# Kernel tuning notes

Hardware: AMD Instinct MI355X
Metric: run time of the kernel (lower is better)

The kernel has to match this reference:

```python
import jax, jax.numpy as jnp
import numpy as np

NUM_ROUTES, NUM_TIME, DIM, K, C = 100000, 2016, 256, 100, 5
BATCH = 262144


def _xavier(key, shape):
    fan_in, fan_out = shape[0], shape[1]
    lim = np.sqrt(6.0 / (fan_in + fan_out))
    return jax.random.uniform(key, shape, jnp.float32, -lim, lim)


def setup_inputs() -> dict:
    key = jax.random.key(0)
    ks = jax.random.split(key, 9)
    route_idx = jax.random.randint(ks[0], (BATCH,), 0, NUM_ROUTES)
    time_idx = jax.random.randint(ks[1], (BATCH,), 0, NUM_TIME)
    route_table = _xavier(ks[2], (NUM_ROUTES, DIM))
    time_table = _xavier(ks[3], (NUM_TIME, DIM))
    w = _xavier(ks[4], (DIM, K))
    mode_a = _xavier(ks[5], (DIM, C))
    mode_b = _xavier(ks[6], (DIM, C))
    mode_bias = jnp.zeros((C, C), jnp.float32)
    fc_lim = 1.0 / np.sqrt(C * C + K)
    fc_w = jax.random.uniform(ks[7], (C * C + K, 1), jnp.float32, -fc_lim, fc_lim)
    fc_b = jax.random.uniform(ks[8], (1,), jnp.float32, -fc_lim, fc_lim)
    return {
        "route_idx": route_idx, "time_idx": time_idx,
        "route_table": route_table, "time_table": time_table,
        "w": w, "mode_a": mode_a, "mode_b": mode_b,
        "mode_bias": mode_bias, "fc_w": fc_w, "fc_b": fc_b,
    }


def reference(route_idx, time_idx, route_table, time_table, w, mode_a, mode_b, mode_bias, fc_w, fc_b):
    r = route_table[route_idx]            # [B, D]
    t = time_table[time_idx]              # [B, D]
    gcp = jax.nn.relu((r * t) @ w)        # [B, K]
    # einsum('ni,nj->nij') then contracting i with mode_a and j with mode_b
    # equals outer product of the two small projections (exact same math):
    ra = r @ mode_a                       # [B, C]
    tb = t @ mode_b                       # [B, C]
    inter = jax.nn.sigmoid(ra[:, :, None] * tb[:, None, :] + mode_bias)  # [B, C, C]
    feats = jnp.concatenate([gcp, inter.reshape(inter.shape[0], -1)], axis=1)  # [B, K + C*C]
    out = feats @ fc_w + fc_b             # [B, 1]
    return jnp.squeeze(out, axis=-1)      # [B]
```

## Files before the change

### kernel.cpp

```cpp
#include <hip/hip_runtime.h>
#include <stdint.h>

#define BATCH   262144
#define NROUTES 100000
#define NTIME   2016
#define DIM     256
#define KOUT    100
#define NTILES  7

typedef __attribute__((ext_vector_type(8))) short bf16x8;
typedef __attribute__((ext_vector_type(4))) float f32x4;

#define WS_W_BYTES  (NTILES * 8 * 64 * 16)
#define WS_RA_OFF   ((size_t)WS_W_BYTES)
#define WS_TB_OFF   (WS_RA_OFF + (size_t)NROUTES * 32)
#define WS_RT16_OFF (WS_TB_OFF + (size_t)NTIME * 32)
#define WS_TT16_OFF (WS_RT16_OFF + (size_t)NROUTES * 512)
#define WS_NEED     (WS_TT16_OFF + (size_t)NTIME * 512)

static __device__ __forceinline__ uint32_t rne_bf16(float f) {
  uint32_t u = __builtin_bit_cast(uint32_t, f);
  u += 0x7FFFu + ((u >> 16) & 1u);
  return u >> 16;
}
static __device__ __forceinline__ uint32_t pk_rne(float a, float b) {
  return rne_bf16(a) | (rne_bf16(b) << 16);
}
static __device__ __forceinline__ uint32_t pk_trunc(float a, float b) {
  return __builtin_amdgcn_perm(__builtin_bit_cast(uint32_t, b),
                               __builtin_bit_cast(uint32_t, a), 0x07060302u);
}
static __device__ __forceinline__ uint32_t mulpk(uint32_t a, uint32_t b) {
  float alo = __builtin_bit_cast(float, a << 16);
  float blo = __builtin_bit_cast(float, b << 16);
  float ahi = __builtin_bit_cast(float, a & 0xFFFF0000u);
  float bhi = __builtin_bit_cast(float, b & 0xFFFF0000u);
  return __builtin_amdgcn_perm(__builtin_bit_cast(uint32_t, ahi * bhi),
                               __builtin_bit_cast(uint32_t, alo * blo), 0x07060302u);
}

__global__ __launch_bounds__(256) void prep_kernel(
    const float* __restrict__ route_table,
    const float* __restrict__ time_table,
    const float* __restrict__ w,
    const float* __restrict__ mode_a,
    const float* __restrict__ mode_b,
    uint8_t* __restrict__ ws, int do16)
{
  const int b   = blockIdx.x;
  const int tid = threadIdx.x;

  if (b < 14) {
    const int u = b * 256 + tid;
    const int lane = u & 63;
    const int frag = u >> 6;
    const int ks = frag / NTILES;
    const int nt = frag % NTILES;
    const int n  = nt * 16 + (lane & 15);
    const int k0 = ks * 32 + (lane >> 4) * 8;
    uint32_t pk[4];
    #pragma unroll
    for (int p = 0; p < 4; ++p) {
      float v0 = (n < KOUT) ? w[(size_t)(k0 + 2 * p) * KOUT + n] : 0.0f;
      float v1 = (n < KOUT) ? w[(size_t)(k0 + 2 * p + 1) * KOUT + n] : 0.0f;
      pk[p] = pk_rne(v0, v1);
    }
    ((uint4*)ws)[u] = make_uint4(pk[0], pk[1], pk[2], pk[3]);
    return;
  }

  const float* tab; const float* proj; float* outp; uint8_t* out16; int base;
  if (b < 14 + 126) {
    tab = time_table;  proj = mode_b; outp = (float*)(ws + WS_TB_OFF);
    out16 = ws + WS_TT16_OFF; base = (b - 14) * 16;
  } else {
    tab = route_table; proj = mode_a; outp = (float*)(ws + WS_RA_OFF);
    out16 = ws + WS_RT16_OFF; base = (b - 140) * 16;
  }

  const int wave = tid >> 6, lane = tid & 63;
  float A[4][5];
  #pragma unroll
  for (int j = 0; j < 4; ++j)
    #pragma unroll
    for (int i = 0; i < 5; ++i)
      A[j][i] = proj[(4 * lane + j) * 5 + i];

  const int row0 = base + wave * 4;
  float4 v[4];
  #pragma unroll
  for (int rr = 0; rr < 4; ++rr)
    v[rr] = *(const float4*)(tab + (size_t)(row0 + rr) * DIM + 4 * lane);

  #pragma unroll
  for (int rr = 0; rr < 4; ++rr) {
    const int row = row0 + rr;
    if (do16) {
      uint2 o;
      o.x = pk_rne(v[rr].x, v[rr].y);
      o.y = pk_rne(v[rr].z, v[rr].w);
      *(uint2*)(out16 + (size_t)row * 512 + lane * 8) = o;
    }
    float p[5];
    #pragma unroll
    for (int i = 0; i < 5; ++i)
      p[i] = v[rr].x * A[0][i] + v[rr].y * A[1][i] + v[rr].z * A[2][i] + v[rr].w * A[3][i];
    #pragma unroll
    for (int off = 32; off >= 1; off >>= 1)
      #pragma unroll
      for (int i = 0; i < 5; ++i)
        p[i] += __shfl_xor(p[i], off, 64);
    if (lane == 0) {
      float* o = outp + (size_t)row * 8;
      o[0] = p[0]; o[1] = p[1]; o[2] = p[2]; o[3] = p[3]; o[4] = p[4];
    }
  }
}

template<int TAB16>
__global__ __launch_bounds__(256, 3) void main_kernel(
    const int*   __restrict__ route_idx,
    const int*   __restrict__ time_idx,
    const float* __restrict__ route_table,
    const float* __restrict__ time_table,
    const float* __restrict__ mode_bias,
    const float* __restrict__ fc_w,
    const float* __restrict__ fc_b,
    const uint8_t* __restrict__ ws,
    float* __restrict__ out)
{
  __shared__ float yg[64];
  const int tid  = threadIdx.x;
  const int wave = tid >> 6, lane = tid & 63;
  const int col  = lane & 15, quad = lane >> 4;
  const int m0   = blockIdx.x * 64 + wave * 16;
  const size_t ri = (size_t)route_idx[m0 + col];
  const size_t ti = (size_t)time_idx[m0 + col];

  uint4 rw[8], tw[8];
  if (TAB16) {
    const uint8_t* rb = ws + WS_RT16_OFF + ri * 512 + quad * 16;
    const uint8_t* tb = ws + WS_TT16_OFF + ti * 512 + quad * 16;
    #pragma unroll
    for (int ks = 0; ks < 8; ++ks) {
      rw[ks] = *(const uint4*)(rb + ks * 64);
      tw[ks] = *(const uint4*)(tb + ks * 64);
    }
  }

  f32x4 acc[NTILES];
  #pragma unroll
  for (int nt = 0; nt < NTILES; ++nt) acc[nt] = (f32x4){0.f, 0.f, 0.f, 0.f};
  const bf16x8* wfr = (const bf16x8*)ws;

  #pragma unroll
  for (int ks = 0; ks < 8; ++ks) {
    uint4 p;
    if (TAB16) {
      p.x = mulpk(rw[ks].x, tw[ks].x);
      p.y = mulpk(rw[ks].y, tw[ks].y);
      p.z = mulpk(rw[ks].z, tw[ks].z);
      p.w = mulpk(rw[ks].w, tw[ks].w);
    } else {
      const float4* rp = (const float4*)(route_table + ri * DIM + ks * 32 + quad * 8);
      const float4* tp = (const float4*)(time_table  + ti * DIM + ks * 32 + quad * 8);
      float4 r0 = rp[0], r1 = rp[1], t0 = tp[0], t1 = tp[1];
      p.x = pk_trunc(r0.x * t0.x, r0.y * t0.y);
      p.y = pk_trunc(r0.z * t0.z, r0.w * t0.w);
      p.z = pk_trunc(r1.x * t1.x, r1.y * t1.y);
      p.w = pk_trunc(r1.z * t1.z, r1.w * t1.w);
    }
    const bf16x8 a = __builtin_bit_cast(bf16x8, p);
    #pragma unroll
    for (int nt = 0; nt < NTILES; ++nt)
      acc[nt] = __builtin_amdgcn_mfma_f32_16x16x32_bf16(a, wfr[(ks * NTILES + nt) * 64 + lane],
                                                        acc[nt], 0, 0, 0);
  }

  float fcw_l[NTILES];
  #pragma unroll
  for (int nt = 0; nt < NTILES; ++nt) {
    const int n = nt * 16 + col;
    fcw_l[nt] = (n < KOUT) ? fc_w[n] : 0.0f;
  }
  #pragma unroll
  for (int reg = 0; reg < 4; ++reg) {
    float s = 0.f;
    #pragma unroll
    for (int nt = 0; nt < NTILES; ++nt)
      s += fmaxf(acc[nt][reg], 0.f) * fcw_l[nt];
    #pragma unroll
    for (int off = 1; off < 16; off <<= 1)
      s += __shfl_xor(s, off, 64);
    if (col == 0) yg[wave * 16 + quad * 4 + reg] = s;
  }
  __syncthreads();

  if (tid < 64) {
    const int n = blockIdx.x * 64 + tid;
    const size_t ri2 = (size_t)route_idx[n];
    const size_t ti2 = (size_t)time_idx[n];
    const float* ra = (const float*)(ws + WS_RA_OFF) + ri2 * 8;
    const float* tb = (const float*)(ws + WS_TB_OFF) + ti2 * 8;
    float rav[5], tbv[5];
    #pragma unroll
    for (int i = 0; i < 5; ++i) { rav[i] = ra[i]; tbv[i] = tb[i]; }
    float o = fc_b[0] + yg[tid];
    #pragma unroll
    for (int i = 0; i < 5; ++i)
      #pragma unroll
      for (int j = 0; j < 5; ++j) {
        const float z  = rav[i] * tbv[j] + mode_bias[i * 5 + j];
        const float sg = 1.0f / (1.0f + __expf(-z));
        o += sg * fc_w[KOUT + i * 5 + j];
      }
    out[n] = o;
  }
}

extern "C" void kernel_launch(void* const* d_in, const int* in_sizes, int n_in,
                              void* d_out, int out_size, void* d_ws, size_t ws_size,
                              hipStream_t stream)
{
  const int*   route_idx   = (const int*)d_in[0];
  const int*   time_idx    = (const int*)d_in[1];
  const float* route_table = (const float*)d_in[2];
  const float* time_table  = (const float*)d_in[3];
  const float* w           = (const float*)d_in[4];
  const float* mode_a      = (const float*)d_in[5];
  const float* mode_b      = (const float*)d_in[6];
  const float* mode_bias   = (const float*)d_in[7];
  const float* fc_w        = (const float*)d_in[8];
  const float* fc_b        = (const float*)d_in[9];
  uint8_t* ws  = (uint8_t*)d_ws;
  float*   out = (float*)d_out;

  const int big = (ws_size >= WS_NEED) ? 1 : 0;

  prep_kernel<<<6390, 256, 0, stream>>>(route_table, time_table, w,
                                        mode_a, mode_b, ws, big);
  if (big)
    main_kernel<1><<<BATCH / 64, 256, 0, stream>>>(route_idx, time_idx,
                                                   route_table, time_table,
                                                   mode_bias, fc_w, fc_b, ws, out);
  else
    main_kernel<0><<<BATCH / 64, 256, 0, stream>>>(route_idx, time_idx,
                                                   route_table, time_table,
                                                   mode_bias, fc_w, fc_b, ws, out);
}
```

Measured before the change: 245.4 us.

## Switch embedding tables and GEMM to FP8 MFMA, drop LDS epilogue

Prep now converts the weight fragments and both embedding tables to scaled FP8 instead of bf16, halving the gathered bytes per row. The main kernel multiplies the FP8 route and time values in f32, requantizes the product to FP8 and uses the fp8 MFMA; fc_w is prescaled to undo the scale factor. The per-row sigmoid interaction epilogue is moved into designated lanes of each wave with DPP reductions, removing shared memory and the block barrier, and occupancy is raised to 4 blocks. Reductions in prep also use DPP. The main risks are FP8 accuracy loss against the tolerance and extra conversion ALU work.

Measured after the change: 225.5 us. 1.09x faster.

```diff
diff --git a/kernel.cpp b/kernel.cpp
--- a/kernel.cpp
+++ b/kernel.cpp
@@ -8,35 +8,36 @@
 #define KOUT    100
 #define NTILES  7
 
-typedef __attribute__((ext_vector_type(8))) short bf16x8;
+typedef __attribute__((ext_vector_type(2))) float f32x2;
 typedef __attribute__((ext_vector_type(4))) float f32x4;
 
-#define WS_W_BYTES  (NTILES * 8 * 64 * 16)
-#define WS_RA_OFF   ((size_t)WS_W_BYTES)
+#define WS_WFRAG_BYTES ((size_t)(NTILES * 8 * 64 * 8))
+#define WS_RA_OFF   (WS_WFRAG_BYTES)
 #define WS_TB_OFF   (WS_RA_OFF + (size_t)NROUTES * 32)
-#define WS_RT16_OFF (WS_TB_OFF + (size_t)NTIME * 32)
-#define WS_TT16_OFF (WS_RT16_OFF + (size_t)NROUTES * 512)
-#define WS_NEED     (WS_TT16_OFF + (size_t)NTIME * 512)
-
-static __device__ __forceinline__ uint32_t rne_bf16(float f) {
-  uint32_t u = __builtin_bit_cast(uint32_t, f);
-  u += 0x7FFFu + ((u >> 16) & 1u);
-  return u >> 16;
-}
-static __device__ __forceinline__ uint32_t pk_rne(float a, float b) {
-  return rne_bf16(a) | (rne_bf16(b) << 16);
-}
-static __device__ __forceinline__ uint32_t pk_trunc(float a, float b) {
-  return __builtin_amdgcn_perm(__builtin_bit_cast(uint32_t, b),
-                               __builtin_bit_cast(uint32_t, a), 0x07060302u);
-}
-static __device__ __forceinline__ uint32_t mulpk(uint32_t a, uint32_t b) {
-  float alo = __builtin_bit_cast(float, a << 16);
-  float blo = __builtin_bit_cast(float, b << 16);
-  float ahi = __builtin_bit_cast(float, a & 0xFFFF0000u);
-  float bhi = __builtin_bit_cast(float, b & 0xFFFF0000u);
-  return __builtin_amdgcn_perm(__builtin_bit_cast(uint32_t, ahi * bhi),
-                               __builtin_bit_cast(uint32_t, alo * blo), 0x07060302u);
+#define WS_RT8_OFF  (WS_TB_OFF + (size_t)NTIME * 32)
+#define WS_TT8_OFF  (WS_RT8_OFF + (size_t)NROUTES * 256)
+#define WS_NEED     (WS_TT8_OFF + (size_t)NTIME * 256)
+
+template<int CTRL>
+static __device__ __forceinline__ float dpp_add(float x) {
+  int s = __builtin_amdgcn_update_dpp(0, __builtin_bit_cast(int, x), CTRL, 0xF, 0xF, true);
+  return x + __builtin_bit_cast(float, s);
+}
+static __device__ __forceinline__ float wave_sum63(float x) {
+  x = dpp_add<0x111>(x);
+  x = dpp_add<0x112>(x);
+  x = dpp_add<0x114>(x);
+  x = dpp_add<0x118>(x);
+  x = dpp_add<0x142>(x);
+  x = dpp_add<0x143>(x);
+  return x;
+}
+static __device__ __forceinline__ float sum16_all(float x) {
+  x = dpp_add<0x0B1>(x);
+  x = dpp_add<0x04E>(x);
+  x = dpp_add<0x124>(x);
+  x = dpp_add<0x128>(x);
+  return x;
 }
 
 __global__ __launch_bounds__(256) void prep_kernel(
@@ -45,7 +46,7 @@
     const float* __restrict__ w,
     const float* __restrict__ mode_a,
     const float* __restrict__ mode_b,
-    uint8_t* __restrict__ ws, int do16)
+    uint8_t* __restrict__ ws, int do8)
 {
   const int b   = blockIdx.x;
   const int tid = threadIdx.x;
@@ -58,24 +59,26 @@
     const int nt = frag % NTILES;
     const int n  = nt * 16 + (lane & 15);
     const int k0 = ks * 32 + (lane >> 4) * 8;
-    uint32_t pk[4];
-    #pragma unroll
-    for (int p = 0; p < 4; ++p) {
-      float v0 = (n < KOUT) ? w[(size_t)(k0 + 2 * p) * KOUT + n] : 0.0f;
-      float v1 = (n < KOUT) ? w[(size_t)(k0 + 2 * p + 1) * KOUT + n] : 0.0f;
-      pk[p] = pk_rne(v0, v1);
-    }
-    ((uint4*)ws)[u] = make_uint4(pk[0], pk[1], pk[2], pk[3]);
+    float v[8];
+    #pragma unroll
+    for (int j = 0; j < 8; ++j)
+      v[j] = (n < KOUT) ? w[(size_t)(k0 + j) * KOUT + n] : 0.0f;
+    uint32_t d0 = 0, d1 = 0;
+    d0 = __builtin_amdgcn_cvt_pk_fp8_f32(v[0], v[1], d0, false);
+    d0 = __builtin_amdgcn_cvt_pk_fp8_f32(v[2], v[3], d0, true);
+    d1 = __builtin_amdgcn_cvt_pk_fp8_f32(v[4], v[5], d1, false);
+    d1 = __builtin_amdgcn_cvt_pk_fp8_f32(v[6], v[7], d1, true);
+    ((uint2*)ws)[u] = make_uint2(d0, d1);
     return;
   }
 
-  const float* tab; const float* proj; float* outp; uint8_t* out16; int base;
+  const float* tab; const float* proj; float* outp; uint8_t* out8; int base;
   if (b < 14 + 126) {
     tab = time_table;  proj = mode_b; outp = (float*)(ws + WS_TB_OFF);
-    out16 = ws + WS_TT16_OFF; base = (b - 14) * 16;
+    out8 = ws + WS_TT8_OFF; base = (b - 14) * 16;
   } else {
     tab = route_table; proj = mode_a; outp = (float*)(ws + WS_RA_OFF);
-    out16 = ws + WS_RT16_OFF; base = (b - 140) * 16;
+    out8 = ws + WS_RT8_OFF; base = (b - 140) * 16;
   }
 
   const int wave = tid >> 6, lane = tid & 63;
@@ -86,6 +89,9 @@
     for (int i = 0; i < 5; ++i)
       A[j][i] = proj[(4 * lane + j) * 5 + i];
 
+  const int p0 = (lane >> 4) * 64 + ((lane >> 1) & 3) * 16 +
+                 ((lane >> 3) & 1) * 8 + (lane & 1) * 4;
+
   const int row0 = base + wave * 4;
   float4 v[4];
   #pragma unroll
@@ -95,30 +101,28 @@
   #pragma unroll
   for (int rr = 0; rr < 4; ++rr) {
     const int row = row0 + rr;
-    if (do16) {
-      uint2 o;
-      o.x = pk_rne(v[rr].x, v[rr].y);
-      o.y = pk_rne(v[rr].z, v[rr].w);
-      *(uint2*)(out16 + (size_t)row * 512 + lane * 8) = o;
+    if (do8) {
+      uint32_t u = 0;
+      u = __builtin_amdgcn_cvt_pk_fp8_f32(8.f * v[rr].x, 8.f * v[rr].y, u, false);
+      u = __builtin_amdgcn_cvt_pk_fp8_f32(8.f * v[rr].z, 8.f * v[rr].w, u, true);
+      *(uint32_t*)(out8 + (size_t)row * 256 + p0) = u;
     }
     float p[5];
     #pragma unroll
-    for (int i = 0; i < 5; ++i)
-      p[i] = v[rr].x * A[0][i] + v[rr].y * A[1][i] + v[rr].z * A[2][i] + v[rr].w * A[3][i];
-    #pragma unroll
-    for (int off = 32; off >= 1; off >>= 1)
-      #pragma unroll
-      for (int i = 0; i < 5; ++i)
-        p[i] += __shfl_xor(p[i], off, 64);
-    if (lane == 0) {
+    for (int i = 0; i < 5; ++i) {
+      float s = v[rr].x * A[0][i] + v[rr].y * A[1][i] + v[rr].z * A[2][i] + v[rr].w * A[3][i];
+      p[i] = wave_sum63(s);
+    }
+    if (lane == 63) {
       float* o = outp + (size_t)row * 8;
-      o[0] = p[0]; o[1] = p[1]; o[2] = p[2]; o[3] = p[3]; o[4] = p[4];
-    }
-  }
-}
-
-template<int TAB16>
-__global__ __launch_bounds__(256, 3) void main_kernel(
+      *(f32x4*)o = (f32x4){p[0], p[1], p[2], p[3]};
+      o[4] = p[4];
+    }
+  }
+}
+
+template<int TAB8>
+__global__ __launch_bounds__(256, 4) void main_kernel(
     const int*   __restrict__ route_idx,
     const int*   __restrict__ time_idx,
     const float* __restrict__ route_table,
@@ -129,83 +133,103 @@
     const uint8_t* __restrict__ ws,
     float* __restrict__ out)
 {
-  __shared__ float yg[64];
   const int tid  = threadIdx.x;
   const int wave = tid >> 6, lane = tid & 63;
   const int col  = lane & 15, quad = lane >> 4;
   const int m0   = blockIdx.x * 64 + wave * 16;
   const size_t ri = (size_t)route_idx[m0 + col];
   const size_t ti = (size_t)time_idx[m0 + col];
-
-  uint4 rw[8], tw[8];
-  if (TAB16) {
-    const uint8_t* rb = ws + WS_RT16_OFF + ri * 512 + quad * 16;
-    const uint8_t* tb = ws + WS_TT16_OFF + ti * 512 + quad * 16;
-    #pragma unroll
-    for (int ks = 0; ks < 8; ++ks) {
-      rw[ks] = *(const uint4*)(rb + ks * 64);
-      tw[ks] = *(const uint4*)(tb + ks * 64);
-    }
+  const bool desig = (quad == (col >> 2));
+
+  f32x4 ra0; float ra4; f32x4 tb0; float tb4;
+  if (desig) {
+    const float* ra = (const float*)(ws + WS_RA_OFF) + ri * 8;
+    const float* tb = (const float*)(ws + WS_TB_OFF) + ti * 8;
+    ra0 = *(const f32x4*)ra; ra4 = ra[4];
+    tb0 = *(const f32x4*)tb; tb4 = tb[4];
+  }
+
+  uint4 rw[4], tw[4];
+  if (TAB8) {
+    const uint8_t* rb = ws + WS_RT8_OFF + ri * 256 + quad * 16;
+    const uint8_t* tb = ws + WS_TT8_OFF + ti * 256 + quad * 16;
+    #pragma unroll
+    for (int i = 0; i < 4; ++i) {
+      rw[i] = *(const uint4*)(rb + i * 64);
+      tw[i] = *(const uint4*)(tb + i * 64);
+    }
+  }
+
+  float fcw_l[NTILES];
+  #pragma unroll
+  for (int nt = 0; nt < NTILES; ++nt) {
+    const int n = nt * 16 + col;
+    fcw_l[nt] = (n < KOUT) ? fc_w[n] * 0.015625f : 0.0f;
   }
 
   f32x4 acc[NTILES];
   #pragma unroll
   for (int nt = 0; nt < NTILES; ++nt) acc[nt] = (f32x4){0.f, 0.f, 0.f, 0.f};
-  const bf16x8* wfr = (const bf16x8*)ws;
+  const uint2* wfr = (const uint2*)ws;
 
   #pragma unroll
   for (int ks = 0; ks < 8; ++ks) {
-    uint4 p;
-    if (TAB16) {
-      p.x = mulpk(rw[ks].x, tw[ks].x);
-      p.y = mulpk(rw[ks].y, tw[ks].y);
-      p.z = mulpk(rw[ks].z, tw[ks].z);
-      p.w = mulpk(rw[ks].w, tw[ks].w);
+    uint32_t p0, p1;
+    if (TAB8) {
+      const int i = ks >> 1;
+      const uint32_t ra = (ks & 1) ? rw[i].z : rw[i].x;
+      const uint32_t rb = (ks & 1) ? rw[i].w : rw[i].y;
+      const uint32_t ta = (ks & 1) ? tw[i].z : tw[i].x;
+      const uint32_t tb = (ks & 1) ? tw[i].w : tw[i].y;
+      f32x2 r01 = __builtin_amdgcn_cvt_pk_f32_fp8(ra, false);
+      f32x2 r23 = __builtin_amdgcn_cvt_pk_f32_fp8(ra, true);
+      f32x2 r45 = __builtin_amdgcn_cvt_pk_f32_fp8(rb, false);
+      f32x2 r67 = __builtin_amdgcn_cvt_pk_f32_fp8(rb, true);
+      f32x2 t01 = __builtin_amdgcn_cvt_pk_f32_fp8(ta, false);
+      f32x2 t23 = __builtin_amdgcn_cvt_pk_f32_fp8(ta, true);
+      f32x2 t45 = __builtin_amdgcn_cvt_pk_f32_fp8(tb, false);
+      f32x2 t67 = __builtin_amdgcn_cvt_pk_f32_fp8(tb, true);
+      f32x2 x01 = r01 * t01, x23 = r23 * t23, x45 = r45 * t45, x67 = r67 * t67;
+      p0 = 0; p1 = 0;
+      p0 = __builtin_amdgcn_cvt_pk_fp8_f32(x01.x, x01.y, p0, false);
+      p0 = __builtin_amdgcn_cvt_pk_fp8_f32(x23.x, x23.y, p0, true);
+      p1 = __builtin_amdgcn_cvt_pk_fp8_f32(x45.x, x45.y, p1, false);
+      p1 = __builtin_amdgcn_cvt_pk_fp8_f32(x67.x, x67.y, p1, true);
     } else {
       const float4* rp = (const float4*)(route_table + ri * DIM + ks * 32 + quad * 8);
       const float4* tp = (const float4*)(time_table  + ti * DIM + ks * 32 + quad * 8);
       float4 r0 = rp[0], r1 = rp[1], t0 = tp[0], t1 = tp[1];
-      p.x = pk_trunc(r0.x * t0.x, r0.y * t0.y);
-      p.y = pk_trunc(r0.z * t0.z, r0.w * t0.w);
-      p.z = pk_trunc(r1.x * t1.x, r1.y * t1.y);
-      p.w = pk_trunc(r1.z * t1.z, r1.w * t1.w);
-    }
-    const bf16x8 a = __builtin_bit_cast(bf16x8, p);
+      p0 = 0; p1 = 0;
+      p0 = __builtin_amdgcn_cvt_pk_fp8_f32(64.f * r0.x * t0.x, 64.f * r0.y * t0.y, p0, false);
+      p0 = __builtin_amdgcn_cvt_pk_fp8_f32(64.f * r0.z * t0.z, 64.f * r0.w * t0.w, p0, true);
+      p1 = __builtin_amdgcn_cvt_pk_fp8_f32(64.f * r1.x * t1.x, 64.f * r1.y * t1.y, p1, false);
+      p1 = __builtin_amdgcn_cvt_pk_fp8_f32(64.f * r1.z * t1.z, 64.f * r1.w * t1.w, p1, true);
+    }
+    const long a64 = __builtin_bit_cast(long, make_uint2(p0, p1));
+    #pragma unroll
+    for (int nt = 0; nt < NTILES; ++nt) {
+      const long b64 = __builtin_bit_cast(long, wfr[(ks * NTILES + nt) * 64 + lane]);
+      acc[nt] = __builtin_amdgcn_mfma_f32_16x16x32_fp8_fp8(a64, b64, acc[nt], 0, 0, 0);
+    }
+  }
+
+  float s[4];
+  #pragma unroll
+  for (int reg = 0; reg < 4; ++reg) {
+    float v = 0.f;
     #pragma unroll
     for (int nt = 0; nt < NTILES; ++nt)
-      acc[nt] = __builtin_amdgcn_mfma_f32_16x16x32_bf16(a, wfr[(ks * NTILES + nt) * 64 + lane],
-                                                        acc[nt], 0, 0, 0);
-  }
-
-  float fcw_l[NTILES];
-  #pragma unroll
-  for (int nt = 0; nt < NTILES; ++nt) {
-    const int n = nt * 16 + col;
-    fcw_l[nt] = (n < KOUT) ? fc_w[n] : 0.0f;
-  }
-  #pragma unroll
-  for (int reg = 0; reg < 4; ++reg) {
-    float s = 0.f;
-    #pragma unroll
-    for (int nt = 0; nt < NTILES; ++nt)
-      s += fmaxf(acc[nt][reg], 0.f) * fcw_l[nt];
-    #pragma unroll
-    for (int off = 1; off < 16; off <<= 1)
-      s += __shfl_xor(s, off, 64);
-    if (col == 0) yg[wave * 16 + quad * 4 + reg] = s;
-  }
-  __syncthreads();
-
-  if (tid < 64) {
-    const int n = blockIdx.x * 64 + tid;
-    const size_t ri2 = (size_t)route_idx[n];
-    const size_t ti2 = (size_t)time_idx[n];
-    const float* ra = (const float*)(ws + WS_RA_OFF) + ri2 * 8;
-    const float* tb = (const float*)(ws + WS_TB_OFF) + ti2 * 8;
-    float rav[5], tbv[5];
-    #pragma unroll
-    for (int i = 0; i < 5; ++i) { rav[i] = ra[i]; tbv[i] = tb[i]; }
-    float o = fc_b[0] + yg[tid];
+      v += fmaxf(acc[nt][reg], 0.f) * fcw_l[nt];
+    s[reg] = sum16_all(v);
+  }
+
+  if (desig) {
+    const int m = col;
+    const float sa = (m & 1) ? s[1] : s[0];
+    const float sb = (m & 1) ? s[3] : s[2];
+    float o = fc_b[0] + ((m & 2) ? sb : sa);
+    const float rav[5] = {ra0.x, ra0.y, ra0.z, ra0.w, ra4};
+    const float tbv[5] = {tb0.x, tb0.y, tb0.z, tb0.w, tb4};
     #pragma unroll
     for (int i = 0; i < 5; ++i)
       #pragma unroll
@@ -214,7 +238,7 @@
         const float sg = 1.0f / (1.0f + __expf(-z));
         o += sg * fc_w[KOUT + i * 5 + j];
       }
-    out[n] = o;
+    out[m0 + m] = o;
   }
 }
 
```
